# Performance work log

Measured on AMD Instinct MI355X. Metric: run time of the kernel, lower is better.

The kernel has to match this reference:

```python
import jax, jax.numpy as jnp
import numpy as np

BS, T, D, R = 8, 256, 2048, 4
N, K, G, GS, H = 8192, 64, 512, 16, 64
MOD_IN, MOD_OUT = K + 5, K + 2


def setup_inputs() -> dict:
    key = jax.random.key(0)
    ks = jax.random.split(key, 8)
    cc_signals = jax.random.normal(ks[0], (BS, T, D), dtype=jnp.float32)
    mod_w1 = jax.random.normal(ks[1], (G, MOD_IN, H), dtype=jnp.float32) * (2.0 / (MOD_IN + H)) ** 0.5
    mod_b1 = jnp.zeros((G, H), dtype=jnp.float32)
    mod_w2 = jax.random.normal(ks[2], (G, H, MOD_OUT), dtype=jnp.float32) * 0.01
    mod_b2 = jax.random.normal(ks[3], (G, MOD_OUT), dtype=jnp.float32) * 0.01
    conn_indices = jax.random.randint(ks[4], (N, K), 0, N, dtype=jnp.int32)
    conn_indices = jnp.sort(conn_indices, axis=-1)
    pos = jnp.arange(N, dtype=jnp.float32)
    neuron_id = jnp.stack([jnp.sin(pos * (2 * np.pi / N)), jnp.cos(pos * (2 * np.pi / N))], axis=-1)
    V0 = jax.random.normal(ks[5], (BS, N), dtype=jnp.float32) * 0.1
    activation0 = jax.nn.sigmoid(V0)
    hebbian0 = jnp.zeros((BS, N, K), dtype=jnp.float32)
    decay0 = jnp.full((BS, N), 0.9, dtype=jnp.float32)
    threshold0 = jnp.zeros((BS, N), dtype=jnp.float32)
    return {"cc_signals": cc_signals, "mod_w1": mod_w1, "mod_b1": mod_b1,
            "mod_w2": mod_w2, "mod_b2": mod_b2, "conn_indices": conn_indices,
            "neuron_id": neuron_id, "V0": V0, "activation0": activation0,
            "hebbian0": hebbian0, "decay0": decay0, "threshold0": threshold0}


def _modulator(activation, hebbian, decay, threshold, neuron_id, w1, b1, w2, b2):
    # [BS, N, K+5]
    nid = jnp.broadcast_to(neuron_id[None], (BS, N, 2))
    mod_in = jnp.concatenate([activation[..., None], hebbian, decay[..., None],
                              threshold[..., None], nid], axis=-1)
    x = mod_in.reshape(BS, G, GS, MOD_IN)
    hdn = jnp.tanh(jnp.einsum('bgsi,gih->bgsh', x, w1) + b1[None, :, None, :])
    out = jnp.einsum('bgsh,gho->bgso', hdn, w2) + b2[None, :, None, :]
    out = out.reshape(BS, N, MOD_OUT)
    return out[..., :K], jax.nn.sigmoid(out[..., K]), out[..., K + 1]


def reference(cc_signals, mod_w1, mod_b1, mod_w2, mod_b2, conn_indices, neuron_id,
              V0, activation0, hebbian0, decay0, threshold0):
    w_conn, decay, threshold = _modulator(activation0, hebbian0, decay0, threshold0,
                                          neuron_id, mod_w1, mod_b1, mod_w2, mod_b2)
    inject_all = jnp.repeat(cc_signals, R, axis=-1)  # [BS, T, N]

    def step(carry, inj_t):
        V, act, heb = carry
        nbr = act[:, conn_indices]                       # [BS, N, K] gather
        recv = jnp.sum(nbr * w_conn, axis=-1) + inj_t    # [BS, N]
        V = decay * V + (1.0 - decay) * recv
        act = jax.nn.sigmoid(V - threshold)
        heb = heb + act[..., None] * nbr
        return (V, act, heb), act

    heb_init = jnp.zeros((BS, N, K), dtype=V0.dtype)
    (_, _, _), acts = jax.lax.scan(step, (V0, activation0, heb_init),
                                   jnp.swapaxes(inject_all, 0, 1))
    act_all = jnp.swapaxes(acts, 0, 1)                   # [BS, T, N]
    mem_out = act_all.reshape(BS, T, D, R).mean(axis=-1)  # readout
    return mem_out
```

## Files before the change

### kernel.cpp

```cpp
#include <hip/hip_runtime.h>
#include <hip/hip_fp16.h>
#include <cstdint>
#include <cstddef>

#define BS 8
#define TT 256
#define DD 2048
#define NN 8192
#define KK 64
#define GG 512
#define GSZ 16
#define HH 64
#define MIN_ 69
#define MOUT_ 66
#define NSL 32
#define SLN 256

typedef float    f32x4 __attribute__((ext_vector_type(4)));
typedef uint32_t u32x4 __attribute__((ext_vector_type(4)));

__global__ __launch_bounds__(256) void prep_kernel(
    const int* __restrict__ conn, int* __restrict__ ad_stored,
    unsigned char* __restrict__ inv2)
{
  const int gtid = blockIdx.x * 256 + threadIdx.x;
  const int n    = gtid >> 6;
  const int lane = gtid & 63;
  int idx  = conn[(size_t)n * KK + lane];
  int bank = idx & 31;
  unsigned key = ((unsigned)bank << 6) | (unsigned)lane;
  int rank = 0;
  #pragma unroll
  for (int i = 0; i < 64; ++i) {
    unsigned ki = (unsigned)__shfl((int)key, i);
    rank += (ki < key) ? 1 : 0;
  }
  const int ln = n & 63;
  const int r  = ((ln & 31) * 2 + (ln >> 5)) & 63;
  int j = (rank - r) & 63;
  ad_stored[(size_t)n * KK + j] = idx << 2;
  inv2[(size_t)n * KK + lane]   = (unsigned char)j;
}

__global__ __launch_bounds__(256) void modulator_kernel(
    const float* __restrict__ w1, const float* __restrict__ b1,
    const float* __restrict__ w2, const float* __restrict__ b2,
    const float* __restrict__ act0, const float* __restrict__ heb0,
    const float* __restrict__ dec0, const float* __restrict__ thr0,
    const float* __restrict__ nid, const unsigned char* __restrict__ inv2,
    float* __restrict__ wconn, float* __restrict__ decayB, float* __restrict__ thrB)
{
  const int g = blockIdx.x, tid = threadIdx.x;
  __shared__ float w1s[MIN_ * HH];
  __shared__ float w2s[HH * MOUT_];
  __shared__ float b2s[MOUT_];
  __shared__ float xs[GSZ][MIN_];
  __shared__ float hd[GSZ * HH];

  for (int j = tid; j < MIN_ * HH; j += 256) w1s[j] = w1[(size_t)g * MIN_ * HH + j];
  for (int j = tid; j < HH * MOUT_; j += 256) w2s[j] = w2[(size_t)g * HH * MOUT_ + j];
  if (tid < MOUT_) b2s[tid] = b2[g * MOUT_ + tid];
  const float b1v = b1[g * HH + (tid & 63)];
  const int nbase = g * GSZ;

  for (int b = 0; b < BS; ++b) {
    __syncthreads();
    for (int j = tid; j < GSZ * KK; j += 256) {
      int s = j >> 6, k = j & 63;
      xs[s][1 + k] = heb0[((size_t)(b * NN + nbase + s)) * KK + k];
    }
    if (tid < GSZ) {
      int n = nbase + tid;
      xs[tid][0]  = act0[b * NN + n];
      xs[tid][65] = dec0[b * NN + n];
      xs[tid][66] = thr0[b * NN + n];
      xs[tid][67] = nid[2 * n];
      xs[tid][68] = nid[2 * n + 1];
    }
    __syncthreads();

    #pragma unroll
    for (int rep = 0; rep < 4; ++rep) {
      int s = rep * 4 + (tid >> 6), h = tid & 63;
      float acc = b1v;
      for (int i = 0; i < MIN_; ++i) acc = fmaf(xs[s][i], w1s[i * HH + h], acc);
      hd[s * HH + h] = tanhf(acc);
    }
    __syncthreads();

    for (int j = tid; j < GSZ * MOUT_; j += 256) {
      int s = j / MOUT_, o = j - s * MOUT_;
      float acc = b2s[o];
      for (int h = 0; h < HH; ++h) acc = fmaf(hd[s * HH + h], w2s[h * MOUT_ + o], acc);
      int nn = nbase + s;
      int gidx = b * NN + nn;
      if (o < KK) {
        int jp = inv2[(size_t)nn * KK + o];
        wconn[(size_t)gidx * KK + jp] = acc;
      }
      else if (o == KK) decayB[gidx] = 1.f / (1.f + expf(-acc));
      else              thrB[gidx]   = acc;
    }
  }
}

__global__ __launch_bounds__(256, 1) void scan_kernel(
    const float* __restrict__ cc, const int* __restrict__ ad_stored,
    const float* __restrict__ V0, const float* __restrict__ act0,
    const float* __restrict__ wconn, const float* __restrict__ decayB,
    const float* __restrict__ thrB,
    float* __restrict__ out, uint32_t* actbuf)
{
  const int tid = threadIdx.x;
  const int b   = blockIdx.x & 7;
  const int sl  = blockIdx.x >> 3;
  const int n    = sl * SLN + tid;
  const int gidx = b * NN + n;

  __shared__ float alds[NN];

  f32x4 w4[16];
  int   ad[KK];
  {
    const f32x4* wr = reinterpret_cast<const f32x4*>(wconn + (size_t)gidx * KK);
    #pragma unroll
    for (int j = 0; j < 16; ++j) w4[j] = wr[j];
    const int4* ir = reinterpret_cast<const int4*>(ad_stored + (size_t)n * KK);
    #pragma unroll
    for (int j = 0; j < KK / 4; ++j) {
      int4 v = ir[j];
      ad[4*j+0] = v.x; ad[4*j+1] = v.y;
      ad[4*j+2] = v.z; ad[4*j+3] = v.w;
    }
  }
  float V     = V0[gidx];
  float dec   = decayB[gidx];
  float onemd = 1.f - dec;
  float thr   = thrB[gidx];

  {
    const float4* src = reinterpret_cast<const float4*>(act0 + (size_t)b * NN);
    float4* dst = reinterpret_cast<float4*>(alds);
    #pragma unroll
    for (int j = 0; j < 8; ++j) dst[tid + j * 256] = src[tid + j * 256];
  }
  __syncthreads();

  float inj = cc[((size_t)b * TT) * DD + (n >> 2)];
  const char* abase = reinterpret_cast<const char*>(alds);

  for (int t = 0; t < TT; ++t) {
    float s0 = 0.f, s1 = 0.f, s2 = 0.f, s3 = 0.f;
    #pragma unroll
    for (int j = 0; j < 16; ++j) {
      s0 = fmaf(*reinterpret_cast<const float*>(abase + ad[4*j+0]), w4[j].x, s0);
      s1 = fmaf(*reinterpret_cast<const float*>(abase + ad[4*j+1]), w4[j].y, s1);
      s2 = fmaf(*reinterpret_cast<const float*>(abase + ad[4*j+2]), w4[j].z, s2);
      s3 = fmaf(*reinterpret_cast<const float*>(abase + ad[4*j+3]), w4[j].w, s3);
    }
    float recv = (s0 + s1) + (s2 + s3) + inj;
    V = dec * V + onemd * recv;
    float x = V - thr;
    float a = 1.f / (1.f + expf(-x));

    const int pw = t & 1;

    if (t != TT - 1) {
      uint32_t word = ((uint32_t)(t + 1) << 16) |
                      (uint32_t)__half_as_ushort(__float2half_rn(a));
      uint32_t* dst = actbuf + (size_t)pw * (BS * NN) + gidx;
      asm volatile("global_store_dword %0, %1, off sc0 sc1"
                   :: "v"(dst), "v"(word) : "memory");
    }

    float p = a + __shfl_xor(a, 1);
    p = p + __shfl_xor(p, 2);
    if ((tid & 3) == 0)
      out[((size_t)b * TT + t) * DD + sl * 64 + (tid >> 2)] = 0.25f * p;

    if (t == TT - 1) break;

    inj = cc[((size_t)b * TT + t + 1) * DD + (n >> 2)];

    const uint32_t* src = actbuf + (size_t)pw * (BS * NN) + (size_t)b * NN;
    const uint32_t expect = (uint32_t)(t + 1) << 16;
    u32x4 vals[8];
    for (;;) {
      #pragma unroll
      for (int j = 0; j < 8; ++j) {
        const uint32_t* p4 = src + (tid << 2) + (j << 10);
        asm volatile("global_load_dwordx4 %0, %1, off sc0 sc1"
                     : "=v"(vals[j]) : "v"(p4));
      }
      asm volatile("s_waitcnt vmcnt(0)" ::: "memory");
      uint32_t bad = 0;
      #pragma unroll
      for (int j = 0; j < 8; ++j) {
        bad |= (vals[j].x & 0xFFFF0000u) ^ expect;
        bad |= (vals[j].y & 0xFFFF0000u) ^ expect;
        bad |= (vals[j].z & 0xFFFF0000u) ^ expect;
        bad |= (vals[j].w & 0xFFFF0000u) ^ expect;
      }
      if (bad == 0) break;
    }
    {
      const int base = (tid << 2);
      #pragma unroll
      for (int j = 0; j < 8; ++j) {
        int o = base + (j << 10);
        alds[o + 0] = __half2float(__ushort_as_half((unsigned short)(vals[j].x & 0xFFFFu)));
        alds[o + 1] = __half2float(__ushort_as_half((unsigned short)(vals[j].y & 0xFFFFu)));
        alds[o + 2] = __half2float(__ushort_as_half((unsigned short)(vals[j].z & 0xFFFFu)));
        alds[o + 3] = __half2float(__ushort_as_half((unsigned short)(vals[j].w & 0xFFFFu)));
      }
    }
    __syncthreads();
  }
}

extern "C" void kernel_launch(void* const* d_in, const int* in_sizes, int n_in,
                              void* d_out, int out_size, void* d_ws, size_t ws_size,
                              hipStream_t stream)
{
  const float* cc   = (const float*)d_in[0];
  const float* w1   = (const float*)d_in[1];
  const float* b1   = (const float*)d_in[2];
  const float* w2   = (const float*)d_in[3];
  const float* b2   = (const float*)d_in[4];
  const int*   conn = (const int*)d_in[5];
  const float* nid  = (const float*)d_in[6];
  const float* V0   = (const float*)d_in[7];
  const float* act0 = (const float*)d_in[8];
  const float* heb0 = (const float*)d_in[9];
  const float* dec0 = (const float*)d_in[10];
  const float* thr0 = (const float*)d_in[11];
  float* out = (float*)d_out;

  char* ws = (char*)d_ws;
  float*         wconn  = (float*)ws;
  float*         decayB = (float*)(ws + (size_t)BS * NN * KK * 4);
  float*         thrB   = decayB + BS * NN;
  uint32_t*      actbuf = (uint32_t*)(thrB + BS * NN);
  int*           ad_st  = (int*)(actbuf + 2 * BS * NN);
  unsigned char* inv2   = (unsigned char*)(ad_st + (size_t)NN * KK);

  hipMemsetAsync(actbuf, 0, 2 * BS * NN * sizeof(uint32_t), stream);

  prep_kernel<<<dim3(NN * KK / 256), 256, 0, stream>>>(conn, ad_st, inv2);
  modulator_kernel<<<dim3(GG), 256, 0, stream>>>(w1, b1, w2, b2, act0, heb0, dec0,
                                                 thr0, nid, inv2, wconn, decayB, thrB);
  scan_kernel<<<dim3(BS * NSL), 256, 0, stream>>>(cc, ad_st, V0, act0, wconn,
                                                  decayB, thrB, out, actbuf);
}
```

Measured before the change: 875.7 us.

## Pack activations as paired 12-bit fixed-point values for inter-block exchange

Activations exchanged between blocks each step are quantized to 12-bit fixed point and packed two per 32-bit word with an 8-bit step tag, halving the global polling traffic and LDS size. Neighbour gathers read packed words and extract the right half via a per-connection parity bitmask, with weights prescaled by 1/4095. This trades extra ALU unpacking work in the gather loop and coarser activation precision for less memory and sync traffic per timestep.

```diff
diff --git a/kernel.cpp b/kernel.cpp
--- a/kernel.cpp
+++ b/kernel.cpp
@@ -1,5 +1,4 @@
 #include <hip/hip_runtime.h>
-#include <hip/hip_fp16.h>
 #include <cstdint>
 #include <cstddef>
 
@@ -15,6 +14,7 @@
 #define MOUT_ 66
 #define NSL 32
 #define SLN 256
+#define NW (NN/2)
 
 typedef float    f32x4 __attribute__((ext_vector_type(4)));
 typedef uint32_t u32x4 __attribute__((ext_vector_type(4)));
@@ -27,7 +27,7 @@
   const int n    = gtid >> 6;
   const int lane = gtid & 63;
   int idx  = conn[(size_t)n * KK + lane];
-  int bank = idx & 31;
+  int bank = (idx >> 1) & 31;
   unsigned key = ((unsigned)bank << 6) | (unsigned)lane;
   int rank = 0;
   #pragma unroll
@@ -38,7 +38,7 @@
   const int ln = n & 63;
   const int r  = ((ln & 31) * 2 + (ln >> 5)) & 63;
   int j = (rank - r) & 63;
-  ad_stored[(size_t)n * KK + j] = idx << 2;
+  ad_stored[(size_t)n * KK + j] = ((idx >> 1) << 2) | (idx & 1);
   inv2[(size_t)n * KK + lane]   = (unsigned char)j;
 }
 
@@ -117,14 +117,18 @@
   const int n    = sl * SLN + tid;
   const int gidx = b * NN + n;
 
-  __shared__ float alds[NN];
+  __shared__ uint32_t alds[NW];
 
   f32x4 w4[16];
   int   ad[KK];
+  uint32_t mlo = 0, mhi = 0;
   {
     const f32x4* wr = reinterpret_cast<const f32x4*>(wconn + (size_t)gidx * KK);
     #pragma unroll
-    for (int j = 0; j < 16; ++j) w4[j] = wr[j];
+    for (int j = 0; j < 16; ++j) {
+      f32x4 v = wr[j];
+      w4[j] = v * (1.f / 4095.f);
+    }
     const int4* ir = reinterpret_cast<const int4*>(ad_stored + (size_t)n * KK);
     #pragma unroll
     for (int j = 0; j < KK / 4; ++j) {
@@ -132,17 +136,22 @@
       ad[4*j+0] = v.x; ad[4*j+1] = v.y;
       ad[4*j+2] = v.z; ad[4*j+3] = v.w;
     }
+    #pragma unroll
+    for (int k = 0; k < 32; ++k) { mlo |= (uint32_t)(ad[k] & 1) << k;      ad[k] &= ~1; }
+    #pragma unroll
+    for (int k = 32; k < 64; ++k) { mhi |= (uint32_t)(ad[k] & 1) << (k-32); ad[k] &= ~1; }
   }
   float V     = V0[gidx];
   float dec   = decayB[gidx];
   float onemd = 1.f - dec;
   float thr   = thrB[gidx];
 
-  {
-    const float4* src = reinterpret_cast<const float4*>(act0 + (size_t)b * NN);
-    float4* dst = reinterpret_cast<float4*>(alds);
-    #pragma unroll
-    for (int j = 0; j < 8; ++j) dst[tid + j * 256] = src[tid + j * 256];
+  for (int w = tid; w < NW; w += 256) {
+    float a0 = act0[(size_t)b * NN + 2 * w];
+    float a1 = act0[(size_t)b * NN + 2 * w + 1];
+    uint32_t q0 = (uint32_t)__builtin_rintf(a0 * 4095.f);
+    uint32_t q1 = (uint32_t)__builtin_rintf(a1 * 4095.f);
+    alds[w] = (q1 << 12) | q0;
   }
   __syncthreads();
 
@@ -153,10 +162,22 @@
     float s0 = 0.f, s1 = 0.f, s2 = 0.f, s3 = 0.f;
     #pragma unroll
     for (int j = 0; j < 16; ++j) {
-      s0 = fmaf(*reinterpret_cast<const float*>(abase + ad[4*j+0]), w4[j].x, s0);
-      s1 = fmaf(*reinterpret_cast<const float*>(abase + ad[4*j+1]), w4[j].y, s1);
-      s2 = fmaf(*reinterpret_cast<const float*>(abase + ad[4*j+2]), w4[j].z, s2);
-      s3 = fmaf(*reinterpret_cast<const float*>(abase + ad[4*j+3]), w4[j].w, s3);
+      uint32_t d0 = *reinterpret_cast<const uint32_t*>(abase + ad[4*j+0]);
+      uint32_t d1 = *reinterpret_cast<const uint32_t*>(abase + ad[4*j+1]);
+      uint32_t d2 = *reinterpret_cast<const uint32_t*>(abase + ad[4*j+2]);
+      uint32_t d3 = *reinterpret_cast<const uint32_t*>(abase + ad[4*j+3]);
+      uint32_t sh0, sh1, sh2, sh3;
+      if (4*j+3 < 32) {
+        sh0 = ((mlo >> (4*j+0)) & 1) * 12; sh1 = ((mlo >> (4*j+1)) & 1) * 12;
+        sh2 = ((mlo >> (4*j+2)) & 1) * 12; sh3 = ((mlo >> (4*j+3)) & 1) * 12;
+      } else {
+        sh0 = ((mhi >> (4*j+0-32)) & 1) * 12; sh1 = ((mhi >> (4*j+1-32)) & 1) * 12;
+        sh2 = ((mhi >> (4*j+2-32)) & 1) * 12; sh3 = ((mhi >> (4*j+3-32)) & 1) * 12;
+      }
+      s0 = fmaf((float)((d0 >> sh0) & 0xFFFu), w4[j].x, s0);
+      s1 = fmaf((float)((d1 >> sh1) & 0xFFFu), w4[j].y, s1);
+      s2 = fmaf((float)((d2 >> sh2) & 0xFFFu), w4[j].z, s2);
+      s3 = fmaf((float)((d3 >> sh3) & 0xFFFu), w4[j].w, s3);
     }
     float recv = (s0 + s1) + (s2 + s3) + inj;
     V = dec * V + onemd * recv;
@@ -166,11 +187,14 @@
     const int pw = t & 1;
 
     if (t != TT - 1) {
-      uint32_t word = ((uint32_t)(t + 1) << 16) |
-                      (uint32_t)__half_as_ushort(__float2half_rn(a));
-      uint32_t* dst = actbuf + (size_t)pw * (BS * NN) + gidx;
-      asm volatile("global_store_dword %0, %1, off sc0 sc1"
-                   :: "v"(dst), "v"(word) : "memory");
+      uint32_t aq = (uint32_t)__builtin_rintf(a * 4095.f);
+      uint32_t oq = (uint32_t)__shfl_xor((int)aq, 1);
+      if ((tid & 1) == 0) {
+        uint32_t word = ((uint32_t)(t + 1) << 24) | (oq << 12) | aq;
+        uint32_t* dst = actbuf + (size_t)pw * (BS * NW) + (gidx >> 1);
+        asm volatile("global_store_dword %0, %1, off sc0 sc1"
+                     :: "v"(dst), "v"(word) : "memory");
+      }
     }
 
     float p = a + __shfl_xor(a, 1);
@@ -182,12 +206,12 @@
 
     inj = cc[((size_t)b * TT + t + 1) * DD + (n >> 2)];
 
-    const uint32_t* src = actbuf + (size_t)pw * (BS * NN) + (size_t)b * NN;
-    const uint32_t expect = (uint32_t)(t + 1) << 16;
-    u32x4 vals[8];
+    const uint32_t* src = actbuf + (size_t)pw * (BS * NW) + (size_t)b * NW;
+    const uint32_t tag = (uint32_t)(t + 1);
+    u32x4 vals[4];
     for (;;) {
       #pragma unroll
-      for (int j = 0; j < 8; ++j) {
+      for (int j = 0; j < 4; ++j) {
         const uint32_t* p4 = src + (tid << 2) + (j << 10);
         asm volatile("global_load_dwordx4 %0, %1, off sc0 sc1"
                      : "=v"(vals[j]) : "v"(p4));
@@ -195,24 +219,18 @@
       asm volatile("s_waitcnt vmcnt(0)" ::: "memory");
       uint32_t bad = 0;
       #pragma unroll
-      for (int j = 0; j < 8; ++j) {
-        bad |= (vals[j].x & 0xFFFF0000u) ^ expect;
-        bad |= (vals[j].y & 0xFFFF0000u) ^ expect;
-        bad |= (vals[j].z & 0xFFFF0000u) ^ expect;
-        bad |= (vals[j].w & 0xFFFF0000u) ^ expect;
+      for (int j = 0; j < 4; ++j) {
+        bad |= (vals[j].x >> 24) ^ tag;
+        bad |= (vals[j].y >> 24) ^ tag;
+        bad |= (vals[j].z >> 24) ^ tag;
+        bad |= (vals[j].w >> 24) ^ tag;
       }
       if (bad == 0) break;
     }
     {
-      const int base = (tid << 2);
+      u32x4* dst = reinterpret_cast<u32x4*>(alds);
       #pragma unroll
-      for (int j = 0; j < 8; ++j) {
-        int o = base + (j << 10);
-        alds[o + 0] = __half2float(__ushort_as_half((unsigned short)(vals[j].x & 0xFFFFu)));
-        alds[o + 1] = __half2float(__ushort_as_half((unsigned short)(vals[j].y & 0xFFFFu)));
-        alds[o + 2] = __half2float(__ushort_as_half((unsigned short)(vals[j].z & 0xFFFFu)));
-        alds[o + 3] = __half2float(__ushort_as_half((unsigned short)(vals[j].w & 0xFFFFu)));
-      }
+      for (int j = 0; j < 4; ++j) dst[tid + j * 256] = vals[j];
     }
     __syncthreads();
   }
@@ -241,10 +259,10 @@
   float*         decayB = (float*)(ws + (size_t)BS * NN * KK * 4);
   float*         thrB   = decayB + BS * NN;
   uint32_t*      actbuf = (uint32_t*)(thrB + BS * NN);
-  int*           ad_st  = (int*)(actbuf + 2 * BS * NN);
+  int*           ad_st  = (int*)(actbuf + 2 * BS * NW);
   unsigned char* inv2   = (unsigned char*)(ad_st + (size_t)NN * KK);
 
-  hipMemsetAsync(actbuf, 0, 2 * BS * NN * sizeof(uint32_t), stream);
+  hipMemsetAsync(actbuf, 0, 2 * BS * NW * sizeof(uint32_t), stream);
 
   prep_kernel<<<dim3(NN * KK / 256), 256, 0, stream>>>(conn, ad_st, inv2);
   modulator_kernel<<<dim3(GG), 256, 0, stream>>>(w1, b1, w2, b2, act0, heb0, dec0,
```

New measurement: 775.0 us, median of 2. -11.5%, faster.
